# Performance work log

Measured on AMD Instinct MI355X. Metric: run time of the kernel, lower is better.

Reference implementation:

```python
import jax, jax.numpy as jnp
import numpy as np

TOP_K = 2


def setup_inputs() -> dict:
    key = jax.random.key(0)
    ks = jax.random.split(key, 7)
    B, S, H = 2, 2048, 2048
    E, A, NS = 8, 64, 16384
    x = jax.random.normal(ks[0], (B, S, H), jnp.float32)
    gate_w = jax.random.normal(ks[1], (E, H), jnp.float32) * 0.01  # nn.init std=0.01
    W = jax.random.normal(ks[2], (H, H), jnp.float32) * 0.02       # base FFN weight [out,in]
    atoms = jax.random.normal(ks[3], (A, NS), jnp.float32) * 0.02
    expert_atom_weights = jax.random.normal(ks[4], (E, A), jnp.float32) * 0.1
    importance = jax.random.normal(ks[5], (E, NS), jnp.float32) * 0.1
    mask_idx = jax.random.randint(ks[6], (NS,), 0, H * H, jnp.int32)  # flat positions in W
    return dict(x=x, gate_w=gate_w, W=W, atoms=atoms,
                expert_atom_weights=expert_atom_weights,
                importance=importance, mask_idx=mask_idx)


def reference(x, gate_w, W, atoms, expert_atom_weights, importance, mask_idx):
    B, S, H = x.shape
    xt = x.reshape(-1, H)                       # [T, H] tokens
    # --- SRDERouter ---
    logits = jnp.clip(xt @ gate_w.T, -50.0, 50.0)          # [T, E]
    top_w, top_idx = jax.lax.top_k(logits, TOP_K)          # [T, K]
    rw = jax.nn.softmax(top_w, axis=-1)                    # [T, K]
    # --- SharedDeltaVocabulary + SparseExpert importance ---
    deltas = jax.nn.softmax(expert_atom_weights, axis=-1) @ atoms   # [E, NS]
    weighted = deltas * jax.nn.sigmoid(importance)                  # [E, NS]
    # --- LearnedMaskSelector: flat idx -> (row, col) of W [out, in] ---
    rows = mask_idx // H                                   # output coords [NS]
    cols = mask_idx % H                                    # input coords  [NS]
    # per-token combined sparse delta values over selected positions
    vals = jnp.einsum('tk,tks->ts', rw, weighted[top_idx])  # [T, NS]
    xg = xt[:, cols]                                        # [T, NS] gather of inputs
    # scatter-add products into output rows: y[t, r] += sum_{j: rows[j]=r} xg[t,j]*vals[t,j]
    contrib = jax.ops.segment_sum((xg * vals).T, rows, num_segments=H)  # [H, T]
    out = xt @ W.T + contrib.T                              # base FFN + sparse expert delta
    return out.reshape(B, S, H)
```

## Files before the change

kernel.cpp:

```cpp
#include <hip/hip_runtime.h>
#include <hip/hip_bf16.h>
#include <stdint.h>

#define H       2048
#define LOGH    11
#define T_TOK   4096
#define NEXP    8
#define NATOM   64
#define NS      16384

typedef short bf16x8 __attribute__((ext_vector_type(8)));
typedef float f32x4  __attribute__((ext_vector_type(4)));

__device__ __forceinline__ unsigned short f2bf(float f) {
  union { float f; unsigned u; } c;
  c.f = f;
  c.u += 0x7fff + ((c.u >> 16) & 1);
  return (unsigned short)(c.u >> 16);
}

__global__ __launch_bounds__(256) void prep_kernel(
    const float* __restrict__ x, const float* __restrict__ gate_w,
    const float* __restrict__ W, unsigned short* __restrict__ xb,
    unsigned short* __restrict__ wb, float4* __restrict__ tokInfo) {
  const int b = blockIdx.x;
  if (b >= T_TOK / 4) {
    const int wblk = b - T_TOK / 4;
    const float4* src = reinterpret_cast<const float4*>(W);
#pragma unroll
    for (int p = 0; p < 8; ++p) {
      const int i = (wblk + p * 512) * 256 + threadIdx.x;
      float4 v = src[i];
      ushort4 o;
      o.x = f2bf(v.x); o.y = f2bf(v.y); o.z = f2bf(v.z); o.w = f2bf(v.w);
      *reinterpret_cast<ushort4*>(wb + (size_t)i * 4) = o;
    }
    return;
  }
  const int wv = threadIdx.x >> 6;
  const int lane = threadIdx.x & 63;
  const int t = b * 4 + wv;
  const float4* xr = reinterpret_cast<const float4*>(x + (size_t)t * H);
  unsigned short* xbr = xb + (size_t)t * H;

  float accs[NEXP];
#pragma unroll
  for (int e = 0; e < NEXP; ++e) accs[e] = 0.f;
#pragma unroll
  for (int it = 0; it < 8; ++it) {
    const int j4 = it * 64 + lane;
    float4 xv = xr[j4];
    ushort4 o;
    o.x = f2bf(xv.x); o.y = f2bf(xv.y); o.z = f2bf(xv.z); o.w = f2bf(xv.w);
    *reinterpret_cast<ushort4*>(xbr + (size_t)j4 * 4) = o;
#pragma unroll
    for (int e = 0; e < NEXP; ++e) {
      float4 gv = reinterpret_cast<const float4*>(gate_w + (size_t)e * H)[j4];
      accs[e] = fmaf(xv.x, gv.x, accs[e]);
      accs[e] = fmaf(xv.y, gv.y, accs[e]);
      accs[e] = fmaf(xv.z, gv.z, accs[e]);
      accs[e] = fmaf(xv.w, gv.w, accs[e]);
    }
  }
#pragma unroll
  for (int e = 0; e < NEXP; ++e) {
    float v = accs[e];
#pragma unroll
    for (int off = 32; off > 0; off >>= 1) v += __shfl_down(v, off);
    accs[e] = v;
  }
  if (lane == 0) {
    float lg[NEXP];
#pragma unroll
    for (int e = 0; e < NEXP; ++e) lg[e] = fminf(fmaxf(accs[e], -50.f), 50.f);
    int e0 = 0; float w0 = lg[0];
#pragma unroll
    for (int e = 1; e < NEXP; ++e) { if (lg[e] > w0) { w0 = lg[e]; e0 = e; } }
    int e1 = -1; float w1 = -3.4e38f;
#pragma unroll
    for (int e = 0; e < NEXP; ++e) {
      if (e == e0) continue;
      if (lg[e] > w1) { w1 = lg[e]; e1 = e; }
    }
    const float r1 = expf(w1 - w0);
    float4 ti;
    ti.x = 1.f / (1.f + r1);
    ti.y = r1 / (1.f + r1);
    ti.z = __int_as_float(e0);
    ti.w = __int_as_float(e1);
    tokInfo[t] = ti;
  }
}

__device__ __forceinline__ int sortedFlat(int pos) {
  const int l = pos >> 7, k = pos & 127;
  return ((k >> 2) << 9) | (l << 2) | (k & 3);
}

__global__ __launch_bounds__(1024) void build_sort_kernel(
    const int* __restrict__ mask_idx, const float* __restrict__ eaw,
    int* __restrict__ elemT, int* __restrict__ posOfS, float* __restrict__ pbuf) {
  __shared__ int hist[H];
  __shared__ int base[H];
  __shared__ int wsum[16];
  __shared__ int wexc[16];
  const int tid = threadIdx.x;

  if (tid < NEXP) {
    float v[NATOM];
#pragma unroll
    for (int a = 0; a < NATOM; ++a) v[a] = eaw[tid * NATOM + a];
    float m = v[0];
#pragma unroll
    for (int a = 1; a < NATOM; ++a) m = fmaxf(m, v[a]);
    float ssum = 0.f;
#pragma unroll
    for (int a = 0; a < NATOM; ++a) { v[a] = expf(v[a] - m); ssum += v[a]; }
    const float inv = 1.f / ssum;
#pragma unroll
    for (int a = 0; a < NATOM; ++a) pbuf[tid * NATOM + a] = v[a] * inv;
  }

  hist[tid] = 0;
  hist[tid + 1024] = 0;
  __syncthreads();
  for (int s = tid; s < NS; s += 1024) {
    int r = mask_idx[s] >> LOGH;
    atomicAdd(&hist[r], 1);
  }
  __syncthreads();
  int a = hist[2 * tid], b = hist[2 * tid + 1];
  int ps = a + b;
  const int lane = tid & 63, wid = tid >> 6;
#pragma unroll
  for (int off = 1; off < 64; off <<= 1) {
    int n = __shfl_up(ps, off);
    if (lane >= off) ps += n;
  }
  if (lane == 63) wsum[wid] = ps;
  __syncthreads();
  if (tid == 0) {
    int run = 0;
    for (int w = 0; w < 16; ++w) { wexc[w] = run; run += wsum[w]; }
  }
  __syncthreads();
  int ex = wexc[wid] + ps - (a + b);
  base[2 * tid] = ex;
  base[2 * tid + 1] = ex + a;
  __syncthreads();
  for (int s = tid; s < NS; s += 1024) {
    int m = mask_idx[s];
    int r = m >> LOGH, c = m & (H - 1);
    int pos = atomicAdd(&base[r], 1);
    const int fl = sortedFlat(pos);
    elemT[fl] = (r << LOGH) | c;
    posOfS[s] = fl;
  }
}

__global__ __launch_bounds__(256) void weighted_kernel(
    const float* __restrict__ pbuf, const float* __restrict__ atoms,
    const float* __restrict__ importance, const int* __restrict__ posOfS,
    float* __restrict__ wSortedT) {
  __shared__ float p[NEXP][NATOM];
  const int tid = threadIdx.x;
#pragma unroll
  for (int i = tid; i < NEXP * NATOM; i += 256) (&p[0][0])[i] = pbuf[i];
  __syncthreads();

  const int s = blockIdx.x * 256 + tid;
  const float* as = atoms + s;

  float acc[NEXP];
#pragma unroll
  for (int e = 0; e < NEXP; ++e) acc[e] = 0.f;

#pragma unroll
  for (int ab = 0; ab < 8; ++ab) {
    float v[8];
#pragma unroll
    for (int j = 0; j < 8; ++j) v[j] = as[(size_t)(ab * 8 + j) * NS];
#pragma unroll
    for (int j = 0; j < 8; ++j)
#pragma unroll
      for (int e = 0; e < NEXP; ++e) acc[e] = fmaf(p[e][ab * 8 + j], v[j], acc[e]);
  }

  const int fl = posOfS[s];
#pragma unroll
  for (int e = 0; e < NEXP; ++e) {
    const float imp = importance[(size_t)e * NS + s];
    const float sig = 1.f / (1.f + expf(-imp));
    wSortedT[(size_t)e * NS + fl] = acc[e] * sig;
  }
}

__global__ __launch_bounds__(256) void gemm_kernel(
    const unsigned short* __restrict__ xb, const unsigned short* __restrict__ wb,
    float* __restrict__ out) {
  __shared__ __align__(16) unsigned short aLds[128 * 32];
  __shared__ __align__(16) unsigned short bLds[128 * 32];
  const int tid  = threadIdx.x;
  const int wave = tid >> 6;
  const int lane = tid & 63;
  const int bid = blockIdx.x;
  const int xcd = bid & 7;
  const int j   = bid >> 3;
  const int n_t = (xcd << 1) | (j & 1);
  const int m_t = j >> 1;
  const int m0 = m_t * 128;
  const int n0 = n_t * 128;
  const int wr = wave >> 1;
  const int wc = wave & 1;

  f32x4 acc[4][4];
#pragma unroll
  for (int i = 0; i < 4; ++i)
#pragma unroll
    for (int jj = 0; jj < 4; ++jj)
#pragma unroll
      for (int r = 0; r < 4; ++r) acc[i][jj][r] = 0.f;

  const int srow = lane >> 2;
  const int kcol = (lane & 3) * 8;

  for (int k0 = 0; k0 < H; k0 += 32) {
#pragma unroll
    for (int p = 0; p < 2; ++p) {
      const int g = p * 4 + wave;
      const unsigned short* ga = xb + (size_t)(m0 + g * 16 + srow) * H + k0 + kcol;
      const unsigned short* gb = wb + (size_t)(n0 + g * 16 + srow) * H + k0 + kcol;
      __builtin_amdgcn_global_load_lds(
          (const __attribute__((address_space(1))) unsigned int*)ga,
          (__attribute__((address_space(3))) unsigned int*)(aLds + g * 16 * 32), 16, 0, 0);
      __builtin_amdgcn_global_load_lds(
          (const __attribute__((address_space(1))) unsigned int*)gb,
          (__attribute__((address_space(3))) unsigned int*)(bLds + g * 16 * 32), 16, 0, 0);
    }
    __syncthreads();

    const int kc = (lane >> 4) * 8;
    const int ar = wr * 64 + (lane & 15);
    const int br = wc * 64 + (lane & 15);
    bf16x8 af[4], bfr[4];
#pragma unroll
    for (int i = 0; i < 4; ++i)
      af[i] = *reinterpret_cast<const bf16x8*>(aLds + (ar + i * 16) * 32 + kc);
#pragma unroll
    for (int jj = 0; jj < 4; ++jj)
      bfr[jj] = *reinterpret_cast<const bf16x8*>(bLds + (br + jj * 16) * 32 + kc);
#pragma unroll
    for (int i = 0; i < 4; ++i)
#pragma unroll
      for (int jj = 0; jj < 4; ++jj)
        acc[i][jj] = __builtin_amdgcn_mfma_f32_16x16x32_bf16(af[i], bfr[jj], acc[i][jj], 0, 0, 0);
    __syncthreads();
  }

  const int cr = (lane >> 4) * 4;
  const int cc = lane & 15;
#pragma unroll
  for (int i = 0; i < 4; ++i)
#pragma unroll
    for (int jj = 0; jj < 4; ++jj)
#pragma unroll
      for (int r = 0; r < 4; ++r)
        out[(size_t)(m0 + wr * 64 + i * 16 + cr + r) * H + (n0 + wc * 64 + jj * 16 + cc)] =
            acc[i][jj][r];
}

__global__ __launch_bounds__(512) void scatter_kernel(
    const float* __restrict__ x, const float* __restrict__ wSortedT,
    const int* __restrict__ elemT, const float4* __restrict__ tokInfo,
    float* __restrict__ out) {
  __shared__ float xrow[4][H];
  __shared__ float acc[4][H];
  const int tid  = threadIdx.x;
  const int tk   = tid >> 7;
  const int l    = tid & 127;
  const int t0   = blockIdx.x * 4;

  {
    const float4* xsrc = reinterpret_cast<const float4*>(x + (size_t)t0 * H);
    float4* xdst = reinterpret_cast<float4*>(&xrow[0][0]);
    float4* adst = reinterpret_cast<float4*>(&acc[0][0]);
    float4 z; z.x = z.y = z.z = z.w = 0.f;
#pragma unroll
    for (int i = 0; i < 4; ++i) {
      xdst[tid + i * 512] = xsrc[tid + i * 512];
      adst[tid + i * 512] = z;
    }
  }
  __syncthreads();

  const int t = t0 + tk;
  const float4 ti = tokInfo[t];
  const float rw0 = ti.x, rw1 = ti.y;
  const int e0 = __float_as_int(ti.z);
  const int e1 = __float_as_int(ti.w);

  const int4*   ev4 = reinterpret_cast<const int4*>(elemT);
  const float4* w04 = reinterpret_cast<const float4*>(wSortedT + (size_t)e0 * NS);
  const float4* w14 = reinterpret_cast<const float4*>(wSortedT + (size_t)e1 * NS);
  float* xw = &xrow[tk][0];
  float* aw = &acc[tk][0];

  float accv = 0.f;
  int curR = -1;
  int flushed = 0;

  int4   ev = ev4[l];
  float4 a  = w04[l];
  float4 b  = w14[l];

#define PROC1(EV, AV, BV, GV)                                     \
  {                                                               \
    const int r = (EV) >> LOGH;                                   \
    const float ct = (GV) * fmaf(rw0, (AV), rw1 * (BV));          \
    if (r != curR) {                                              \
      if (curR >= 0) {                                            \
        if (flushed) aw[curR] = accv;                             \
        else { atomicAdd(&aw[curR], accv); flushed = 1; }         \
      }                                                           \
      curR = r; accv = ct;                                        \
    } else {                                                      \
      accv += ct;                                                 \
    }                                                             \
  }

#pragma unroll 4
  for (int s = 0; s < 32; ++s) {
    const int sn = (s + 1 <= 31) ? s + 1 : 31;
    int4   evN = ev4[sn * 128 + l];
    float4 aN  = w04[sn * 128 + l];
    float4 bN  = w14[sn * 128 + l];
    const float g0 = xw[ev.x & (H - 1)];
    const float g1 = xw[ev.y & (H - 1)];
    const float g2 = xw[ev.z & (H - 1)];
    const float g3 = xw[ev.w & (H - 1)];
    PROC1(ev.x, a.x, b.x, g0)
    PROC1(ev.y, a.y, b.y, g1)
    PROC1(ev.z, a.z, b.z, g2)
    PROC1(ev.w, a.w, b.w, g3)
    ev = evN; a = aN; b = bN;
  }
  atomicAdd(&aw[curR], accv);
  __syncthreads();
#undef PROC1

  {
    float4* orow = reinterpret_cast<float4*>(out + (size_t)t * H);
    const float4* arow = reinterpret_cast<const float4*>(aw);
#pragma unroll
    for (int i = 0; i < 4; ++i) {
      int idx = l + i * 128;
      float4 o = orow[idx];
      float4 av = arow[idx];
      o.x += av.x; o.y += av.y; o.z += av.z; o.w += av.w;
      orow[idx] = o;
    }
  }
}

extern "C" void kernel_launch(void* const* d_in, const int* in_sizes, int n_in,
                              void* d_out, int out_size, void* d_ws, size_t ws_size,
                              hipStream_t stream) {
  const float* x          = (const float*)d_in[0];
  const float* gate_w     = (const float*)d_in[1];
  const float* W          = (const float*)d_in[2];
  const float* atoms      = (const float*)d_in[3];
  const float* eaw        = (const float*)d_in[4];
  const float* importance = (const float*)d_in[5];
  const int*   mask_idx   = (const int*)d_in[6];
  float* out = (float*)d_out;

  char* ws = (char*)d_ws;
  size_t off = 0;
  unsigned short* xb = (unsigned short*)(ws + off); off += (size_t)T_TOK * H * 2;
  unsigned short* wb = (unsigned short*)(ws + off); off += (size_t)H * H * 2;
  float4* tokInfo    = (float4*)(ws + off);         off += (size_t)T_TOK * 16;
  int* elemT         = (int*)(ws + off);            off += (size_t)NS * 4;
  int* posOfS        = (int*)(ws + off);            off += (size_t)NS * 4;
  float* wSortedT    = (float*)(ws + off);          off += (size_t)NEXP * NS * 4;
  float* pbuf        = (float*)(ws + off);          off += (size_t)NEXP * NATOM * 4;

  prep_kernel<<<T_TOK / 4 + 512, 256, 0, stream>>>(x, gate_w, W, xb, wb, tokInfo);
  build_sort_kernel<<<1, 1024, 0, stream>>>(mask_idx, eaw, elemT, posOfS, pbuf);
  weighted_kernel<<<NS / 256, 256, 0, stream>>>(pbuf, atoms, importance, posOfS, wSortedT);
  gemm_kernel<<<512, 256, 0, stream>>>(xb, wb, out);
  scatter_kernel<<<T_TOK / 4, 512, 0, stream>>>(x, wSortedT, elemT, tokInfo, out);
}
```

Measured before the change: 242.0 us.

## Double-buffer GEMM LDS tiles, remap block tiling, read bf16 x in scatter

The GEMM now uses two LDS buffers so the global-to-LDS load of the next K tile is issued before the MFMAs on the current tile, with one barrier per step instead of two. The block-to-tile mapping is changed so each XCD covers a 4x8 patch of output tiles, which is meant to improve L2 reuse of A and B. The scatter kernel reads the bf16 copy of x instead of the fp32 original, halving that read traffic. Using bf16 x for the sparse delta term adds rounding error compared with the fp32 reference.

After: 242.5 us. About the same (+0.2%).

```diff
diff --git a/kernel.cpp b/kernel.cpp
--- a/kernel.cpp
+++ b/kernel.cpp
@@ -198,16 +198,16 @@
 __global__ __launch_bounds__(256) void gemm_kernel(
     const unsigned short* __restrict__ xb, const unsigned short* __restrict__ wb,
     float* __restrict__ out) {
-  __shared__ __align__(16) unsigned short aLds[128 * 32];
-  __shared__ __align__(16) unsigned short bLds[128 * 32];
+  __shared__ __align__(16) unsigned short aLds[2][128 * 32];
+  __shared__ __align__(16) unsigned short bLds[2][128 * 32];
   const int tid  = threadIdx.x;
   const int wave = tid >> 6;
   const int lane = tid & 63;
   const int bid = blockIdx.x;
   const int xcd = bid & 7;
   const int j   = bid >> 3;
-  const int n_t = (xcd << 1) | (j & 1);
-  const int m_t = j >> 1;
+  const int m_t = ((xcd >> 1) << 3) | (j >> 3);
+  const int n_t = ((xcd & 1) << 3) | (j & 7);
   const int m0 = m_t * 128;
   const int n0 = n_t * 128;
   const int wr = wave >> 1;
@@ -221,41 +221,58 @@
 #pragma unroll
       for (int r = 0; r < 4; ++r) acc[i][jj][r] = 0.f;
 
-  const int srow = lane >> 2;
-  const int kcol = (lane & 3) * 8;
-
-  for (int k0 = 0; k0 < H; k0 += 32) {
-#pragma unroll
-    for (int p = 0; p < 2; ++p) {
-      const int g = p * 4 + wave;
-      const unsigned short* ga = xb + (size_t)(m0 + g * 16 + srow) * H + k0 + kcol;
-      const unsigned short* gb = wb + (size_t)(n0 + g * 16 + srow) * H + k0 + kcol;
-      __builtin_amdgcn_global_load_lds(
-          (const __attribute__((address_space(1))) unsigned int*)ga,
-          (__attribute__((address_space(3))) unsigned int*)(aLds + g * 16 * 32), 16, 0, 0);
-      __builtin_amdgcn_global_load_lds(
-          (const __attribute__((address_space(1))) unsigned int*)gb,
-          (__attribute__((address_space(3))) unsigned int*)(bLds + g * 16 * 32), 16, 0, 0);
-    }
-    __syncthreads();
-
-    const int kc = (lane >> 4) * 8;
-    const int ar = wr * 64 + (lane & 15);
-    const int br = wc * 64 + (lane & 15);
+#define STAGE(buf, k0)                                                          \
+  {                                                                             \
+    _Pragma("unroll")                                                           \
+    for (int p = 0; p < 2; ++p) {                                               \
+      const int flat = p * 256 + tid;                                           \
+      const int row = flat >> 2;                                                \
+      const int c8 = (flat & 3) * 8;                                            \
+      __builtin_amdgcn_global_load_lds(                                         \
+          (const __attribute__((address_space(1))) unsigned int*)               \
+              (xb + (size_t)(m0 + row) * H + (k0) + c8),                        \
+          (__attribute__((address_space(3))) unsigned int*)                     \
+              (&aLds[buf][flat * 8]), 16, 0, 0);                                \
+      __builtin_amdgcn_global_load_lds(                                         \
+          (const __attribute__((address_space(1))) unsigned int*)               \
+              (wb + (size_t)(n0 + row) * H + (k0) + c8),                        \
+          (__attribute__((address_space(3))) unsigned int*)                     \
+              (&bLds[buf][flat * 8]), 16, 0, 0);                                \
+    }                                                                           \
+  }
+
+  STAGE(0, 0)
+  asm volatile("s_waitcnt vmcnt(0)" ::: "memory");
+  __builtin_amdgcn_s_barrier();
+  __builtin_amdgcn_sched_barrier(0);
+
+  const int kc = (lane >> 4) * 8;
+  const int ar = wr * 64 + (lane & 15);
+  const int br = wc * 64 + (lane & 15);
+
+  for (int kt = 0; kt < 64; ++kt) {
+    const int cur = kt & 1;
+    if (kt < 63) STAGE(cur ^ 1, (kt + 1) * 32)
+
     bf16x8 af[4], bfr[4];
 #pragma unroll
     for (int i = 0; i < 4; ++i)
-      af[i] = *reinterpret_cast<const bf16x8*>(aLds + (ar + i * 16) * 32 + kc);
+      af[i] = *reinterpret_cast<const bf16x8*>(&aLds[cur][(ar + i * 16) * 32 + kc]);
 #pragma unroll
     for (int jj = 0; jj < 4; ++jj)
-      bfr[jj] = *reinterpret_cast<const bf16x8*>(bLds + (br + jj * 16) * 32 + kc);
+      bfr[jj] = *reinterpret_cast<const bf16x8*>(&bLds[cur][(br + jj * 16) * 32 + kc]);
 #pragma unroll
     for (int i = 0; i < 4; ++i)
 #pragma unroll
       for (int jj = 0; jj < 4; ++jj)
         acc[i][jj] = __builtin_amdgcn_mfma_f32_16x16x32_bf16(af[i], bfr[jj], acc[i][jj], 0, 0, 0);
-    __syncthreads();
-  }
+
+    __builtin_amdgcn_sched_barrier(0);
+    asm volatile("s_waitcnt vmcnt(0) lgkmcnt(0)" ::: "memory");
+    __builtin_amdgcn_s_barrier();
+    __builtin_amdgcn_sched_barrier(0);
+  }
+#undef STAGE
 
   const int cr = (lane >> 4) * 4;
   const int cc = lane & 15;
@@ -270,7 +287,7 @@
 }
 
 __global__ __launch_bounds__(512) void scatter_kernel(
-    const float* __restrict__ x, const float* __restrict__ wSortedT,
+    const unsigned short* __restrict__ xb, const float* __restrict__ wSortedT,
     const int* __restrict__ elemT, const float4* __restrict__ tokInfo,
     float* __restrict__ out) {
   __shared__ float xrow[4][H];
@@ -281,15 +298,28 @@
   const int t0   = blockIdx.x * 4;
 
   {
-    const float4* xsrc = reinterpret_cast<const float4*>(x + (size_t)t0 * H);
+    const uint4* xsrc = reinterpret_cast<const uint4*>(xb + (size_t)t0 * H);
     float4* xdst = reinterpret_cast<float4*>(&xrow[0][0]);
     float4* adst = reinterpret_cast<float4*>(&acc[0][0]);
     float4 z; z.x = z.y = z.z = z.w = 0.f;
 #pragma unroll
-    for (int i = 0; i < 4; ++i) {
-      xdst[tid + i * 512] = xsrc[tid + i * 512];
-      adst[tid + i * 512] = z;
+    for (int i = 0; i < 2; ++i) {
+      const int idx = tid + i * 512;
+      uint4 v = xsrc[idx];
+      float4 f0, f1;
+      f0.x = __uint_as_float(v.x << 16);
+      f0.y = __uint_as_float(v.x & 0xffff0000u);
+      f0.z = __uint_as_float(v.y << 16);
+      f0.w = __uint_as_float(v.y & 0xffff0000u);
+      f1.x = __uint_as_float(v.z << 16);
+      f1.y = __uint_as_float(v.z & 0xffff0000u);
+      f1.z = __uint_as_float(v.w << 16);
+      f1.w = __uint_as_float(v.w & 0xffff0000u);
+      xdst[idx * 2]     = f0;
+      xdst[idx * 2 + 1] = f1;
     }
+#pragma unroll
+    for (int i = 0; i < 4; ++i) adst[tid + i * 512] = z;
   }
   __syncthreads();
 
@@ -388,5 +418,5 @@
   build_sort_kernel<<<1, 1024, 0, stream>>>(mask_idx, eaw, elemT, posOfS, pbuf);
   weighted_kernel<<<NS / 256, 256, 0, stream>>>(pbuf, atoms, importance, posOfS, wSortedT);
   gemm_kernel<<<512, 256, 0, stream>>>(xb, wb, out);
-  scatter_kernel<<<T_TOK / 4, 512, 0, stream>>>(x, wSortedT, elemT, tokInfo, out);
-}
+  scatter_kernel<<<T_TOK / 4, 512, 0, stream>>>(xb, wSortedT, elemT, tokInfo, out);
+}
```
